# Performance work log

Measured on AMD Instinct MI355X. Metric: run time of the kernel, lower is better.

The kernel has to match this reference:

```python
import jax, jax.numpy as jnp
import numpy as np

# FlowNetC correlation hyperparameters (kernel_size=1, stride1=1, corr_multiply=1)
PAD = 20          # pad_size
MD = 20           # max_displacement
STRIDE2 = 2       # displacement stride
D = 2 * MD // STRIDE2 + 1  # 21 displacements per axis -> D*D = 441 output channels


def setup_inputs() -> dict:
    key = jax.random.key(0)
    k1, k2 = jax.random.split(key)
    B, C, H, W = 8, 256, 96, 128
    input1 = jax.random.normal(k1, (B, C, H, W), dtype=jnp.float32)
    input2 = jax.random.normal(k2, (B, C, H, W), dtype=jnp.float32)
    return {"input1": input1, "input2": input2}


def _correlation(input1, input2):
    """FlowNet correlation: out[b, d, y, x] = mean_c in1[b,c,y,x] * in2p[b,c,y+oy,x+ox]
    where (oy, ox) enumerate the 21x21 displacement grid (stride2=2) over the
    zero-padded second feature map. Normalization is by C (kernel_size=1)."""
    B, C, H, W = input1.shape
    in2p = jnp.pad(input2, ((0, 0), (0, 0), (PAD, PAD), (PAD, PAD)))

    def one_displacement(idx):
        oy = (idx // D) * STRIDE2  # 0..2*MD, corresponds to dy = oy - MD
        ox = (idx % D) * STRIDE2
        sl = jax.lax.dynamic_slice(in2p, (0, 0, oy, ox), (B, C, H, W))
        return jnp.mean(input1 * sl, axis=1)  # [B, H, W]

    # lax.map keeps only one shifted slice live at a time (avoids a
    # [441, B, C, H, W] intermediate that vmap would materialize).
    out = jax.lax.map(one_displacement, jnp.arange(D * D))  # [D*D, B, H, W]
    return jnp.transpose(out, (1, 0, 2, 3))  # [B, D*D, H, W]


def reference(input1, input2):
    return _correlation(input1, input2)
```

## Files before the change

### kernel.cpp

```cpp
#include <hip/hip_runtime.h>
#include <hip/hip_bf16.h>


typedef short short8 __attribute__((ext_vector_type(8)));
typedef float f32x4 __attribute__((ext_vector_type(4)));

#define IN1T_BYTES 50331648ull
#define WS_NEEDED 125829120ull

__device__ __forceinline__ unsigned short f2bf(float f) {
  union { float f; unsigned int u; } v; v.f = f;
  unsigned int u = v.u;
  u += 0x7fffu + ((u >> 16) & 1u);
  return (unsigned short)(u >> 16);
}

__device__ __forceinline__ void gload16(const unsigned short* g, unsigned short* l) {
  __builtin_amdgcn_global_load_lds((__attribute__((address_space(1))) unsigned int*)g,
                                   (__attribute__((address_space(3))) unsigned int*)l,
                                   16, 0, 0);
}

__global__ __launch_bounds__(256) void t1_kernel(const float* __restrict__ in1,
                                                 unsigned short* __restrict__ in1t) {
  __shared__ float sm[64][129];
  int bid = blockIdx.x;
  int cchunk = bid & 3;
  int t = bid >> 2;
  int y = t % 96;
  int b = t / 96;
  int c0 = cchunk * 64;
  for (int i = threadIdx.x; i < 64 * 128; i += 256) {
    int cl = i >> 7, x = i & 127;
    sm[cl][x] = in1[(((size_t)(b * 256 + c0 + cl)) * 96 + y) * 128 + x];
  }
  __syncthreads();
  size_t obase = ((size_t)(b * 96 + y)) * (2 * 64 * 256);
  for (int u = threadIdx.x; u < 1024; u += 256) {
    int p = u >> 9, m = (u >> 3) & 63, cb = u & 7;
    int x = p + 2 * m;
    short8 w;
#pragma unroll
    for (int e = 0; e < 8; ++e) w[e] = (short)f2bf(sm[cb * 8 + e][x]);
    size_t o = obase + ((size_t)(p * 64 + m)) * 256 + c0 + ((cb ^ (m & 7)) << 3);
    *reinterpret_cast<short8*>(in1t + o) = w;
  }
}

__global__ __launch_bounds__(256) void t2_kernel(const float* __restrict__ in2,
                                                 unsigned short* __restrict__ in2t) {
  __shared__ float sm[64][129];
  int bid = blockIdx.x;
  int cchunk = bid & 3;
  int t = bid >> 2;
  int y2 = t % 96;
  int b = t / 96;
  int c0 = cchunk * 64;
  for (int i = threadIdx.x; i < 64 * 128; i += 256) {
    int cl = i >> 7, x = i & 127;
    sm[cl][x] = in2[(((size_t)(b * 256 + c0 + cl)) * 96 + y2) * 128 + x];
  }
  __syncthreads();
  size_t obase = ((size_t)(b * 96 + y2)) * (2 * 96 * 256);
  for (int u = threadIdx.x; u < 1536; u += 256) {
    int p = u / 768;
    int r = u % 768;
    int k = r >> 3, cb = r & 7;
    int x2 = p + 2 * k - 20;
    bool ok = (unsigned)x2 < 128u;
    short8 w;
#pragma unroll
    for (int e = 0; e < 8; ++e) w[e] = ok ? (short)f2bf(sm[cb * 8 + e][x2]) : (short)0;
    size_t o = obase + ((size_t)(p * 96 + k)) * 256 + c0 + ((cb ^ (k & 7)) << 3);
    *reinterpret_cast<short8*>(in2t + o) = w;
  }
}

__global__ __launch_bounds__(256) void corr_kernel(const unsigned short* __restrict__ in1t,
                                                   const unsigned short* __restrict__ in2t,
                                                   float* __restrict__ out) {
  __shared__ unsigned short ldsA[2][128][64];
  __shared__ unsigned short ldsB[2][192][64];

  int bid = blockIdx.x;
  int wg = (bid & 7) * 2016 + (bid >> 3);
  int b = wg / 2016;
  int r0 = wg % 2016;
  int y = r0 / 21;
  int dyi = r0 % 21;
  int y2 = y + 2 * dyi - 20;
  int tid = threadIdx.x;

  if ((unsigned)y2 >= 96u) {
    f32x4 z = {0.f, 0.f, 0.f, 0.f};
    for (int i = tid; i < 672; i += 256) {
      int oxi = i >> 5, xq = i & 31;
      size_t o = (((size_t)(b * 441 + dyi * 21 + oxi)) * 96 + y) * 128 + xq * 4;
      *reinterpret_cast<f32x4*>(out + o) = z;
    }
    return;
  }

  int lane = tid & 63;
  int wid = tid >> 6;
  int p = wid & 1, cs = wid >> 1;

  size_t baseA = ((size_t)(b * 96 + y)) * 32768;
  size_t baseB = ((size_t)(b * 96 + y2)) * 49152;

  int i8 = lane >> 3, seg = lane & 7;

  auto stage = [&](int buf, int n) {
    int c0 = n * 64;
    for (int t = wid; t < 40; t += 4) {
      if (t < 16) {
        const unsigned short* g = in1t + baseA + (size_t)(t * 8 + i8) * 256 + c0 + seg * 8;
        unsigned short* l = &ldsA[buf][0][0] + t * 512 + lane * 8;
        gload16(g, l);
      } else {
        int j = t - 16;
        const unsigned short* g = in2t + baseB + (size_t)(j * 8 + i8) * 256 + c0 + seg * 8;
        unsigned short* l = &ldsB[buf][0][0] + j * 512 + lane * 8;
        gload16(g, l);
      }
    }
  };

  f32x4 acc[12];
#pragma unroll
  for (int t = 0; t < 12; ++t) acc[t] = (f32x4){0.f, 0.f, 0.f, 0.f};

  int ml = lane & 15, g4 = lane >> 4, q = lane & 7;
  int blk8 = ((cs * 4 + g4) ^ q) * 8;

  stage(0, 0);
  __syncthreads();

  for (int n = 0; n < 4; ++n) {
    if (n < 3) stage((n + 1) & 1, n + 1);
    int buf = n & 1;
    const unsigned short* lA = &ldsA[buf][p * 64][0];
    const unsigned short* lB = &ldsB[buf][p * 96][0];
    short8 af[4], bfr[6];
#pragma unroll
    for (int mt = 0; mt < 4; ++mt)
      af[mt] = *reinterpret_cast<const short8*>(lA + (16 * mt + ml) * 64 + blk8);
#pragma unroll
    for (int nt = 0; nt < 6; ++nt)
      bfr[nt] = *reinterpret_cast<const short8*>(lB + (16 * nt + ml) * 64 + blk8);
#pragma unroll
    for (int mt = 0; mt < 4; ++mt)
#pragma unroll
      for (int jj = 0; jj < 3; ++jj)
        acc[mt * 3 + jj] = __builtin_amdgcn_mfma_f32_16x16x32_bf16(
            af[mt], bfr[mt + jj], acc[mt * 3 + jj], 0, 0, 0);
    __syncthreads();
  }

  float(*eb)[128] = reinterpret_cast<float(*)[128]>(&ldsA[0][0][0]);
  const float sc = 1.0f / 256.0f;
  if (cs == 0) {
#pragma unroll
    for (int mt = 0; mt < 4; ++mt)
#pragma unroll
      for (int jj = 0; jj < 3; ++jj)
#pragma unroll
        for (int r = 0; r < 4; ++r) {
          int mg = 16 * mt + g4 * 4 + r;
          int oxi = 16 * jj + ml - (g4 * 4 + r);
          if ((unsigned)oxi < 21u) eb[oxi][p + 2 * mg] = acc[mt * 3 + jj][r] * sc;
        }
  }
  __syncthreads();
  if (cs == 1) {
#pragma unroll
    for (int mt = 0; mt < 4; ++mt)
#pragma unroll
      for (int jj = 0; jj < 3; ++jj)
#pragma unroll
        for (int r = 0; r < 4; ++r) {
          int mg = 16 * mt + g4 * 4 + r;
          int oxi = 16 * jj + ml - (g4 * 4 + r);
          if ((unsigned)oxi < 21u) eb[oxi][p + 2 * mg] += acc[mt * 3 + jj][r] * sc;
        }
  }
  __syncthreads();
  for (int i = tid; i < 672; i += 256) {
    int oxi = i >> 5, xq = i & 31;
    size_t o = (((size_t)(b * 441 + dyi * 21 + oxi)) * 96 + y) * 128 + xq * 4;
    f32x4 v = *reinterpret_cast<f32x4*>(&eb[oxi][xq * 4]);
    *reinterpret_cast<f32x4*>(out + o) = v;
  }
}

__global__ __launch_bounds__(256) void corr_fallback(const float* __restrict__ in1,
                                                     const float* __restrict__ in2,
                                                     float* __restrict__ out) {
  __shared__ float s1[64][129];
  __shared__ float s2[64][129];
  int bid = blockIdx.x;
  int b = bid / 2016;
  int r0 = bid % 2016;
  int y = r0 / 21;
  int dyi = r0 % 21;
  int y2 = y + 2 * dyi - 20;
  int tid = threadIdx.x;
  bool rowvalid = (unsigned)y2 < 96u;

  float acc[11];
#pragma unroll
  for (int j = 0; j < 11; ++j) acc[j] = 0.f;

  if (rowvalid) {
    for (int cc = 0; cc < 4; ++cc) {
      int c0 = cc * 64;
      __syncthreads();
      for (int i = tid; i < 8192; i += 256) {
        int c = i >> 7, x = i & 127;
        s1[c][x] = in1[(((size_t)(b * 256 + c0 + c)) * 96 + y) * 128 + x];
        s2[c][x] = in2[(((size_t)(b * 256 + c0 + c)) * 96 + y2) * 128 + x];
      }
      __syncthreads();
#pragma unroll
      for (int j = 0; j < 11; ++j) {
        int idx = j * 256 + tid;
        if (idx < 2688) {
          int oxi = idx >> 7, x = idx & 127;
          int x2 = x + 2 * oxi - 20;
          if ((unsigned)x2 < 128u) {
            float a = 0.f;
            for (int c = 0; c < 64; ++c) a += s1[c][x] * s2[c][x2];
            acc[j] += a;
          }
        }
      }
    }
  }
#pragma unroll
  for (int j = 0; j < 11; ++j) {
    int idx = j * 256 + tid;
    if (idx < 2688) {
      int oxi = idx >> 7, x = idx & 127;
      out[(((size_t)(b * 441 + dyi * 21 + oxi)) * 96 + y) * 128 + x] = acc[j] * (1.0f / 256.0f);
    }
  }
}

extern "C" void kernel_launch(void* const* d_in, const int* in_sizes, int n_in,
                              void* d_out, int out_size, void* d_ws, size_t ws_size,
                              hipStream_t stream) {
  const float* in1 = (const float*)d_in[0];
  const float* in2 = (const float*)d_in[1];
  float* out = (float*)d_out;

  if (ws_size >= WS_NEEDED) {
    unsigned short* in1t = (unsigned short*)d_ws;
    unsigned short* in2t = (unsigned short*)((char*)d_ws + IN1T_BYTES);
    t1_kernel<<<3072, 256, 0, stream>>>(in1, in1t);
    t2_kernel<<<3072, 256, 0, stream>>>(in2, in2t);
    corr_kernel<<<16128, 256, 0, stream>>>(in1t, in2t, out);
  } else {
    corr_fallback<<<16128, 256, 0, stream>>>(in1, in2, out);
  }
}
```

Baseline: 603.5 us.

## Keep in1 row fragments in registers and loop over all displacements per block

Result: faster. 492.8 us (-18.3%).

```diff
diff --git a/kernel.cpp b/kernel.cpp
--- a/kernel.cpp
+++ b/kernel.cpp
@@ -30,19 +30,21 @@
   int y = t % 96;
   int b = t / 96;
   int c0 = cchunk * 64;
-  for (int i = threadIdx.x; i < 64 * 128; i += 256) {
-    int cl = i >> 7, x = i & 127;
-    sm[cl][x] = in1[(((size_t)(b * 256 + c0 + cl)) * 96 + y) * 128 + x];
+  for (int i = threadIdx.x; i < 2048; i += 256) {
+    int cl = i >> 5, xq = (i & 31) << 2;
+    f32x4 v = *reinterpret_cast<const f32x4*>(
+        in1 + (((size_t)(b * 256 + c0 + cl)) * 96 + y) * 128 + xq);
+    sm[cl][xq] = v[0]; sm[cl][xq + 1] = v[1]; sm[cl][xq + 2] = v[2]; sm[cl][xq + 3] = v[3];
   }
   __syncthreads();
-  size_t obase = ((size_t)(b * 96 + y)) * (2 * 64 * 256);
+  size_t obase = ((size_t)(b * 96 + y)) * 32768;
   for (int u = threadIdx.x; u < 1024; u += 256) {
     int p = u >> 9, m = (u >> 3) & 63, cb = u & 7;
     int x = p + 2 * m;
     short8 w;
 #pragma unroll
     for (int e = 0; e < 8; ++e) w[e] = (short)f2bf(sm[cb * 8 + e][x]);
-    size_t o = obase + ((size_t)(p * 64 + m)) * 256 + c0 + ((cb ^ (m & 7)) << 3);
+    size_t o = obase + ((size_t)(p * 64 + m)) * 256 + c0 + (cb << 3);
     *reinterpret_cast<short8*>(in1t + o) = w;
   }
 }
@@ -56,12 +58,14 @@
   int y2 = t % 96;
   int b = t / 96;
   int c0 = cchunk * 64;
-  for (int i = threadIdx.x; i < 64 * 128; i += 256) {
-    int cl = i >> 7, x = i & 127;
-    sm[cl][x] = in2[(((size_t)(b * 256 + c0 + cl)) * 96 + y2) * 128 + x];
+  for (int i = threadIdx.x; i < 2048; i += 256) {
+    int cl = i >> 5, xq = (i & 31) << 2;
+    f32x4 v = *reinterpret_cast<const f32x4*>(
+        in2 + (((size_t)(b * 256 + c0 + cl)) * 96 + y2) * 128 + xq);
+    sm[cl][xq] = v[0]; sm[cl][xq + 1] = v[1]; sm[cl][xq + 2] = v[2]; sm[cl][xq + 3] = v[3];
   }
   __syncthreads();
-  size_t obase = ((size_t)(b * 96 + y2)) * (2 * 96 * 256);
+  size_t obase = ((size_t)(b * 96 + y2)) * 49152;
   for (int u = threadIdx.x; u < 1536; u += 256) {
     int p = u / 768;
     int r = u % 768;
@@ -76,120 +80,107 @@
   }
 }
 
-__global__ __launch_bounds__(256) void corr_kernel(const unsigned short* __restrict__ in1t,
-                                                   const unsigned short* __restrict__ in2t,
-                                                   float* __restrict__ out) {
-  __shared__ unsigned short ldsA[2][128][64];
+__global__ __launch_bounds__(256, 3) void corr_kernel(const unsigned short* __restrict__ in1t,
+                                                      const unsigned short* __restrict__ in2t,
+                                                      float* __restrict__ out) {
   __shared__ unsigned short ldsB[2][192][64];
 
   int bid = blockIdx.x;
-  int wg = (bid & 7) * 2016 + (bid >> 3);
-  int b = wg / 2016;
-  int r0 = wg % 2016;
-  int y = r0 / 21;
-  int dyi = r0 % 21;
-  int y2 = y + 2 * dyi - 20;
-  int tid = threadIdx.x;
-
-  if ((unsigned)y2 >= 96u) {
-    f32x4 z = {0.f, 0.f, 0.f, 0.f};
-    for (int i = tid; i < 672; i += 256) {
-      int oxi = i >> 5, xq = i & 31;
-      size_t o = (((size_t)(b * 441 + dyi * 21 + oxi)) * 96 + y) * 128 + xq * 4;
-      *reinterpret_cast<f32x4*>(out + o) = z;
-    }
-    return;
-  }
-
-  int lane = tid & 63;
-  int wid = tid >> 6;
-  int p = wid & 1, cs = wid >> 1;
-
-  size_t baseA = ((size_t)(b * 96 + y)) * 32768;
-  size_t baseB = ((size_t)(b * 96 + y2)) * 49152;
-
-  int i8 = lane >> 3, seg = lane & 7;
-
-  auto stage = [&](int buf, int n) {
-    int c0 = n * 64;
-    for (int t = wid; t < 40; t += 4) {
-      if (t < 16) {
-        const unsigned short* g = in1t + baseA + (size_t)(t * 8 + i8) * 256 + c0 + seg * 8;
-        unsigned short* l = &ldsA[buf][0][0] + t * 512 + lane * 8;
-        gload16(g, l);
-      } else {
-        int j = t - 16;
-        const unsigned short* g = in2t + baseB + (size_t)(j * 8 + i8) * 256 + c0 + seg * 8;
-        unsigned short* l = &ldsB[buf][0][0] + j * 512 + lane * 8;
-        gload16(g, l);
-      }
+  int wg = (bid & 7) * 96 + (bid >> 3);
+  int b = wg / 96, y = wg % 96;
+  int tid = threadIdx.x, lane = tid & 63, wid = tid >> 6;
+  int p = wid & 1, sm2 = wid >> 1;
+  int ml = lane & 15, g4 = lane >> 4, q = lane & 7, i8 = lane >> 3;
+
+  short8 af[2][8];
+  {
+    const unsigned short* Ap = in1t + ((size_t)(b * 96 + y)) * 32768 + (size_t)p * 16384;
+#pragma unroll
+    for (int l = 0; l < 2; ++l) {
+      const unsigned short* Ar = Ap + (size_t)((sm2 * 2 + l) * 16 + ml) * 256 + g4 * 8;
+#pragma unroll
+      for (int ks = 0; ks < 8; ++ks)
+        af[l][ks] = *reinterpret_cast<const short8*>(Ar + ks * 32);
+    }
+  }
+
+  size_t b96y2base = (size_t)(b * 96);
+  auto stage = [&](int y2c, int cc, int buf) {
+    const unsigned short* g = in2t + (b96y2base + y2c) * 49152 + cc * 64 + q * 8;
+    unsigned short* l0 = &ldsB[buf][0][0] + lane * 8;
+#pragma unroll
+    for (int j = 0; j < 6; ++j) {
+      int t = wid * 6 + j;
+      gload16(g + (size_t)(t * 8 + i8) * 256, l0 + t * 512);
     }
   };
-
-  f32x4 acc[12];
-#pragma unroll
-  for (int t = 0; t < 12; ++t) acc[t] = (f32x4){0.f, 0.f, 0.f, 0.f};
-
-  int ml = lane & 15, g4 = lane >> 4, q = lane & 7;
-  int blk8 = ((cs * 4 + g4) ^ q) * 8;
-
-  stage(0, 0);
-  __syncthreads();
-
-  for (int n = 0; n < 4; ++n) {
-    if (n < 3) stage((n + 1) & 1, n + 1);
-    int buf = n & 1;
-    const unsigned short* lA = &ldsA[buf][p * 64][0];
-    const unsigned short* lB = &ldsB[buf][p * 96][0];
-    short8 af[4], bfr[6];
-#pragma unroll
-    for (int mt = 0; mt < 4; ++mt)
-      af[mt] = *reinterpret_cast<const short8*>(lA + (16 * mt + ml) * 64 + blk8);
-#pragma unroll
-    for (int nt = 0; nt < 6; ++nt)
-      bfr[nt] = *reinterpret_cast<const short8*>(lB + (16 * nt + ml) * 64 + blk8);
-#pragma unroll
-    for (int mt = 0; mt < 4; ++mt)
-#pragma unroll
-      for (int jj = 0; jj < 3; ++jj)
-        acc[mt * 3 + jj] = __builtin_amdgcn_mfma_f32_16x16x32_bf16(
-            af[mt], bfr[mt + jj], acc[mt * 3 + jj], 0, 0, 0);
-    __syncthreads();
-  }
-
-  float(*eb)[128] = reinterpret_cast<float(*)[128]>(&ldsA[0][0][0]);
+  auto y2clamp = [&](int d) { int v = y + 2 * d - 20; return ((unsigned)v < 96u) ? v : 0; };
+
+  stage(y2clamp(0), 0, 0);
+
+  f32x4 acc[2][3];
   const float sc = 1.0f / 256.0f;
-  if (cs == 0) {
-#pragma unroll
-    for (int mt = 0; mt < 4; ++mt)
-#pragma unroll
-      for (int jj = 0; jj < 3; ++jj)
-#pragma unroll
-        for (int r = 0; r < 4; ++r) {
-          int mg = 16 * mt + g4 * 4 + r;
-          int oxi = 16 * jj + ml - (g4 * 4 + r);
-          if ((unsigned)oxi < 21u) eb[oxi][p + 2 * mg] = acc[mt * 3 + jj][r] * sc;
+
+  for (int dyi = 0; dyi < 21; ++dyi) {
+    bool valid = ((unsigned)(y + 2 * dyi - 20) < 96u);
+#pragma unroll
+    for (int cc = 0; cc < 4; ++cc) {
+      if (cc == 0) {
+#pragma unroll
+        for (int l = 0; l < 2; ++l)
+#pragma unroll
+          for (int jj = 0; jj < 3; ++jj) acc[l][jj] = (f32x4){0.f, 0.f, 0.f, 0.f};
+      }
+      { int ndyi = dyi + (cc == 3 ? 1 : 0);
+        stage(y2clamp(ndyi), (cc + 1) & 3, (cc + 1) & 1); }
+      asm volatile("s_waitcnt vmcnt(6)" ::: "memory");
+      __builtin_amdgcn_s_barrier();
+      if (valid) {
+#pragma unroll
+        for (int ks = 0; ks < 2; ++ks) {
+          short8 bf[4];
+#pragma unroll
+          for (int t = 0; t < 4; ++t) {
+            int row = p * 96 + (sm2 * 2 + t) * 16 + ml;
+            bf[t] = *reinterpret_cast<const short8*>(
+                &ldsB[cc & 1][0][0] + row * 64 + (((ks * 4 + g4) ^ q) << 3));
+          }
+#pragma unroll
+          for (int l = 0; l < 2; ++l)
+#pragma unroll
+            for (int jj = 0; jj < 3; ++jj)
+              acc[l][jj] = __builtin_amdgcn_mfma_f32_16x16x32_bf16(
+                  af[l][cc * 2 + ks], bf[l + jj], acc[l][jj], 0, 0, 0);
         }
-  }
-  __syncthreads();
-  if (cs == 1) {
-#pragma unroll
-    for (int mt = 0; mt < 4; ++mt)
-#pragma unroll
-      for (int jj = 0; jj < 3; ++jj)
-#pragma unroll
-        for (int r = 0; r < 4; ++r) {
-          int mg = 16 * mt + g4 * 4 + r;
-          int oxi = 16 * jj + ml - (g4 * 4 + r);
-          if ((unsigned)oxi < 21u) eb[oxi][p + 2 * mg] += acc[mt * 3 + jj][r] * sc;
+      }
+      asm volatile("s_waitcnt lgkmcnt(0)" ::: "memory");
+      __builtin_amdgcn_sched_barrier(0);
+      __builtin_amdgcn_s_barrier();
+      if (cc == 3) {
+        if (valid) {
+#pragma unroll
+          for (int l = 0; l < 2; ++l) {
+            int x0 = p + 2 * ((sm2 * 2 + l) * 16 + g4 * 4);
+#pragma unroll
+            for (int jj = 0; jj < 3; ++jj)
+#pragma unroll
+              for (int r = 0; r < 4; ++r) {
+                int oxi = 16 * jj + ml - g4 * 4 - r;
+                if ((unsigned)oxi < 21u)
+                  out[(((size_t)(b * 441 + dyi * 21 + oxi)) * 96 + y) * 128 + x0 + 2 * r] =
+                      acc[l][jj][r] * sc;
+              }
+          }
+        } else {
+          f32x4 z = {0.f, 0.f, 0.f, 0.f};
+          for (int i = tid; i < 672; i += 256) {
+            int oxi = i >> 5, xq = i & 31;
+            *reinterpret_cast<f32x4*>(
+                out + (((size_t)(b * 441 + dyi * 21 + oxi)) * 96 + y) * 128 + xq * 4) = z;
+          }
         }
-  }
-  __syncthreads();
-  for (int i = tid; i < 672; i += 256) {
-    int oxi = i >> 5, xq = i & 31;
-    size_t o = (((size_t)(b * 441 + dyi * 21 + oxi)) * 96 + y) * 128 + xq * 4;
-    f32x4 v = *reinterpret_cast<f32x4*>(&eb[oxi][xq * 4]);
-    *reinterpret_cast<f32x4*>(out + o) = v;
+      }
+    }
   }
 }
 
@@ -258,7 +249,7 @@
     unsigned short* in2t = (unsigned short*)((char*)d_ws + IN1T_BYTES);
     t1_kernel<<<3072, 256, 0, stream>>>(in1, in1t);
     t2_kernel<<<3072, 256, 0, stream>>>(in2, in2t);
-    corr_kernel<<<16128, 256, 0, stream>>>(in1t, in2t, out);
+    corr_kernel<<<768, 256, 0, stream>>>(in1t, in2t, out);
   } else {
     corr_fallback<<<16128, 256, 0, stream>>>(in1, in2, out);
   }
```
